# Kernel optimization log

Hardware: AMD Instinct MI355X
Metric: run time of the kernel (lower is better)

The kernel has to match this reference:

```python
import jax, jax.numpy as jnp
import numpy as np

B, N, C_IN = 4, 2048, 64
HID, HEADS, NQ = 128, 4, 16
D = HID // HEADS  # per-head dim = 32
NEG_SLOPE = 0.2
MASK_VAL = -1e9


def setup_inputs() -> dict:
    key = jax.random.key(0)
    ks = jax.random.split(key, 8)
    x = jax.random.normal(ks[0], (B, N, C_IN), dtype=jnp.float32)
    adj = jax.random.randint(ks[1], (N, N), 0, 2, dtype=jnp.int32)
    # lin_in: Linear(in_channels, hidden_dim)
    W_in = jax.random.normal(ks[2], (C_IN, HID), dtype=jnp.float32) / np.sqrt(C_IN)
    b_in = jnp.zeros((HID,), dtype=jnp.float32)
    # attention vectors [1, heads, d]
    att_src = jax.random.normal(ks[3], (1, HEADS, D), dtype=jnp.float32) * 0.1
    att_dst = jax.random.normal(ks[4], (1, HEADS, D), dtype=jnp.float32) * 0.1
    # output_head: Linear(num_nodes*hidden_dim, num_qubits)
    W_out = jax.random.normal(ks[5], (N * HID, NQ), dtype=jnp.float32) / np.sqrt(N * HID)
    b_out = jnp.zeros((NQ,), dtype=jnp.float32)
    return {"x": x, "adj": adj, "W_in": W_in, "b_in": b_in,
            "att_src": att_src, "att_dst": att_dst,
            "W_out": W_out, "b_out": b_out}


def reference(x, adj, W_in, b_in, att_src, att_dst, W_out, b_out):
    b, n, _ = x.shape
    h = (x @ W_in + b_in).reshape(b, n, HEADS, D)          # [B,N,H,D]
    alpha_src = jnp.sum(h * att_src, axis=-1)               # [B,N,H]
    alpha_dst = jnp.sum(h * att_dst, axis=-1)               # [B,N,H]
    # additive scores: score[b,i,j,h] = src[b,i,h] + dst[b,j,h]
    scores = alpha_src[:, :, None, :] + alpha_dst[:, None, :, :]  # [B,N,N,H]
    scores = jnp.where(scores >= 0, scores, NEG_SLOPE * scores)   # leaky relu
    mask = (adj == 0)[None, :, :, None]                     # [1,N,N,1]
    scores = jnp.where(mask, MASK_VAL, scores)
    alpha = jax.nn.softmax(scores, axis=2)                  # softmax over neighbors j
    # dropout p=0.0 (eval) -> identity
    out = jnp.einsum('bijh,bjhd->bihd', alpha, h)           # [B,N,H,D]
    out = out.reshape(b, n * HEADS * D)                     # [B, N*HID]
    return out @ W_out + b_out                              # [B, NQ]
```

## Files before the change

kernel.cpp:

```cpp
#include <hip/hip_runtime.h>
#include <math.h>

#define BB 4
#define NN 2048
#define CIN 64
#define HID 128
#define HEADS 4
#define NQ 16
#define KTOT (NN*HID)
#define LOG2E 1.44269504088896340736f
#define NEGBIG_BITS 0xC2C80000u
#define NSL 2

typedef __attribute__((ext_vector_type(8))) _Float16 half8;
typedef __attribute__((ext_vector_type(2))) _Float16 half2;
typedef __attribute__((ext_vector_type(4))) float f32x4;
typedef __attribute__((ext_vector_type(4))) unsigned uint4v;

#define GLDS16(g, l) __builtin_amdgcn_global_load_lds((const __attribute__((address_space(1))) unsigned int*)(g), (__attribute__((address_space(3))) unsigned int*)(l), 16, 0, 0)

__global__ __launch_bounds__(256) void k_hidden(
    const float* __restrict__ x, const float* __restrict__ W_in,
    const float* __restrict__ b_in, const float* __restrict__ att_src,
    const float* __restrict__ att_dst, _Float16* __restrict__ hH,
    float* __restrict__ srcA, float* __restrict__ dstA)
{
    __shared__ float Wl[CIN * HID];
    __shared__ float xl[16][CIN];
    const int t = threadIdx.x;
    const int jj0 = blockIdx.x * 16;

    {
        const float4* Ws = (const float4*)W_in;
        float4* Wd = (float4*)Wl;
#pragma unroll
        for (int u = 0; u < 8; ++u) Wd[t + 256 * u] = Ws[t + 256 * u];
        ((float4*)&xl[0][0])[t] = ((const float4*)(x + (size_t)jj0 * CIN))[t];
    }
    __syncthreads();

    const int c = t & 127, rg = t >> 7;
    const int b = jj0 >> 11, j0 = (jj0 & (NN - 1)) + rg * 8;
    const int h = c >> 5;

    float acc[8];
    const float bc = b_in[c];
#pragma unroll
    for (int rr = 0; rr < 8; ++rr) acc[rr] = bc;

#pragma unroll
    for (int k4 = 0; k4 < CIN; k4 += 4) {
        const float w0 = Wl[(k4 + 0) * HID + c];
        const float w1 = Wl[(k4 + 1) * HID + c];
        const float w2 = Wl[(k4 + 2) * HID + c];
        const float w3 = Wl[(k4 + 3) * HID + c];
#pragma unroll
        for (int rr = 0; rr < 8; ++rr) {
            const float4 xv = *(const float4*)&xl[rg * 8 + rr][k4];
            acc[rr] = fmaf(xv.w, w3, fmaf(xv.z, w2, fmaf(xv.y, w1, fmaf(xv.x, w0, acc[rr]))));
        }
    }

    half8 hv;
#pragma unroll
    for (int rr = 0; rr < 8; ++rr) hv[rr] = (_Float16)acc[rr];
    *(half8*)(hH + (size_t)(b * HID + c) * NN + j0) = hv;

    const float as = att_src[c], ad = att_dst[c];
#pragma unroll
    for (int rr = 0; rr < 8; ++rr) {
        float vs = acc[rr] * as, vd = acc[rr] * ad;
#pragma unroll
        for (int m = 16; m >= 1; m >>= 1) {
            vs += __shfl_xor(vs, m, 64);
            vd += __shfl_xor(vd, m, 64);
        }
        if ((t & 31) == 0) {
            srcA[(size_t)(b * HEADS + h) * NN + j0 + rr] = vs * LOG2E;
            dstA[(size_t)(b * HEADS + h) * NN + j0 + rr] = vd * LOG2E;
        }
    }
}

__global__ __launch_bounds__(256) void k_adjb(const int* __restrict__ adj,
                                              unsigned* __restrict__ adjb,
                                              const float* __restrict__ b_out,
                                              float* __restrict__ dout)
{
    const int t = threadIdx.x;
    if (blockIdx.x == 0 && t < 64) dout[t] = b_out[t & 15];
    const int gid = blockIdx.x * 256 + t;
    const int lane = t & 63;
    const int4* p = (const int4*)(adj + (size_t)gid * 8);
    const int4 a = p[0], b = p[1];
    unsigned byte =
        (a.x != 0 ? 1u : 0u)  | (a.y != 0 ? 2u : 0u)  | (a.z != 0 ? 4u : 0u)  | (a.w != 0 ? 8u : 0u) |
        (b.x != 0 ? 16u : 0u) | (b.y != 0 ? 32u : 0u) | (b.z != 0 ? 64u : 0u) | (b.w != 0 ? 128u : 0u);
    unsigned u = byte | (((unsigned)__shfl_xor((int)byte, 1, 64)) << 8);
    u = u | (((unsigned)__shfl_xor((int)u, 2, 64)) << 16);
    if ((lane & 3) == 0) adjb[gid >> 2] = u;
}

__global__ __launch_bounds__(256, 4) void k_attn(
    const unsigned* __restrict__ adjb, const _Float16* __restrict__ hH,
    const float* __restrict__ srcA, const float* __restrict__ dstA,
    float* __restrict__ P, float* __restrict__ S)
{
    __shared__ __align__(16) char sm[4 * 8192];

    const int t = threadIdx.x;
    const int lane = t & 63;
    const int w = t >> 6;
    const int h = w;
    const int bx = blockIdx.x;
    const int ih = bx & 1;
    const int it = (bx >> 1) & 63;
    const int b = (bx >> 7) & 3;
    const int jh = bx >> 9;
    const int i0 = it * 32;
    const int jbase = jh * 1024;

    const int r16 = lane & 15;
    const int g = lane >> 4;
    const int sw16 = (r16 & 7) << 4;

    char* mybuf = sm + w * 8192;
    const _Float16* hrow = hH + ((size_t)(b * HID) + h * 32) * NN;
    const float srci = srcA[(size_t)(b * HEADS + h) * NN + i0 + ih * 16 + r16];
    const uint2* adjr = (const uint2*)(adjb + (size_t)(i0 + ih * 16 + r16) * (NN / 32)) + (jbase >> 6);
    const float4* dstt = (const float4*)(dstA + (size_t)(b * HEADS + h) * NN + jbase);

    const int srow = lane >> 3;
    const int sj8 = (lane & 7) ^ srow;
    auto STAGE = [&](int buf, int n) {
        const int jt = jbase + n * 64;
        const _Float16* gsrc = hrow + (size_t)srow * NN + jt + sj8 * 8;
        char* ldst = mybuf + buf * 4096;
#pragma unroll
        for (int u = 0; u < 4; ++u)
            GLDS16(gsrc + (size_t)(u * 8) * NN, ldst + u * 1024);
    };

    f32x4 acc0 = {0.f, 0.f, 0.f, 0.f};
    f32x4 acc1 = {0.f, 0.f, 0.f, 0.f};
    f32x4 accS = {0.f, 0.f, 0.f, 0.f};
    const half8 ones = {(_Float16)1.f, (_Float16)1.f, (_Float16)1.f, (_Float16)1.f,
                        (_Float16)1.f, (_Float16)1.f, (_Float16)1.f, (_Float16)1.f};

    STAGE(0, 0);
    asm volatile("s_waitcnt vmcnt(0)" ::: "memory");

    int buf = 0;
#pragma unroll 1
    for (int n = 0; n < 16; ++n) {
        if (n + 1 < 16) STAGE(buf ^ 1, n + 1);

        const uint2 aw = adjr[n];
        const char* hb = mybuf + buf * 4096;

#pragma unroll
        for (int jg = 0; jg < 2; ++jg) {
            const int cb = jg * 64 + g * 16;
            const half8 bb0 = *(const half8*)(hb + r16 * 128 + (cb ^ sw16));
            const half8 bb1 = *(const half8*)(hb + (16 + r16) * 128 + (cb ^ sw16));
            const float4 dv0 = dstt[n * 16 + jg * 8 + g * 2];
            const float4 dv1 = dstt[n * 16 + jg * 8 + g * 2 + 1];
            const unsigned bits = (jg ? aw.y : aw.x) >> (8 * g);
            const float dvv[8] = {dv0.x, dv0.y, dv0.z, dv0.w, dv1.x, dv1.y, dv1.z, dv1.w};
            float wv[8];
#pragma unroll
            for (int e = 0; e < 8; ++e) {
                float s = srci + dvv[e];
                s = fmaxf(s, 0.2f * s);
                const unsigned m = (unsigned)(((int)(bits << (31 - e))) >> 31);
                const unsigned su = __builtin_bit_cast(unsigned, s);
                wv[e] = __builtin_amdgcn_exp2f(
                    __builtin_bit_cast(float, (su & m) | (NEGBIG_BITS & ~m)));
            }
            uint4v uu;
            uu[0] = __builtin_bit_cast(unsigned, __builtin_amdgcn_cvt_pkrtz(wv[0], wv[1]));
            uu[1] = __builtin_bit_cast(unsigned, __builtin_amdgcn_cvt_pkrtz(wv[2], wv[3]));
            uu[2] = __builtin_bit_cast(unsigned, __builtin_amdgcn_cvt_pkrtz(wv[4], wv[5]));
            uu[3] = __builtin_bit_cast(unsigned, __builtin_amdgcn_cvt_pkrtz(wv[6], wv[7]));
            const half8 af = __builtin_bit_cast(half8, uu);
            acc0 = __builtin_amdgcn_mfma_f32_16x16x32_f16(af, bb0, acc0, 0, 0, 0);
            acc1 = __builtin_amdgcn_mfma_f32_16x16x32_f16(af, bb1, acc1, 0, 0, 0);
            accS = __builtin_amdgcn_mfma_f32_16x16x32_f16(af, ones, accS, 0, 0, 0);
        }

        asm volatile("s_waitcnt vmcnt(0)" ::: "memory");
        buf ^= 1;
    }

    const size_t prow0 = (size_t)(jh * BB + b) * NN + i0 + ih * 16;
#pragma unroll
    for (int r = 0; r < 4; ++r) {
        const size_t row = prow0 + 4 * g + r;
        P[row * HID + h * 32 + r16]      = acc0[r];
        P[row * HID + h * 32 + 16 + r16] = acc1[r];
        if (r16 == 0) S[row * HEADS + h] = accS[r];
    }
}

__global__ __launch_bounds__(256) void k_proj(
    const float* __restrict__ P, const float* __restrict__ S,
    const float* __restrict__ W_out, float* __restrict__ dout)
{
    __shared__ float wlT[NQ][260];
    __shared__ float red[256];

    const int t = threadIdx.x;
    const int k0 = blockIdx.x * 256;

#pragma unroll
    for (int u = 0; u < 4; ++u) {
        const int flat = (u * 256 + t) * 4;
        const float4 wv = *(const float4*)(W_out + (size_t)k0 * NQ + flat);
        const int krel = flat >> 4;
        const int q0 = flat & 15;
        wlT[q0 + 0][krel] = wv.x;
        wlT[q0 + 1][krel] = wv.y;
        wlT[q0 + 2][krel] = wv.z;
        wlT[q0 + 3][krel] = wv.w;
    }
    __syncthreads();

    const int q = t & 15;
    const int b = (t >> 4) & 3;
    const int ks = (t >> 6) * 64;
    const int i = (k0 + ks) >> 7;

    const float* p0 = P + (size_t)b * KTOT + k0 + ks;
    const float* p1 = P + (size_t)(BB + b) * KTOT + k0 + ks;

    float acc = 0.f;
#pragma unroll
    for (int seg = 0; seg < 2; ++seg) {
        const int h = ((k0 + ks + seg * 32) >> 5) & 3;
        const float rs = S[((size_t)b * NN + i) * HEADS + h] +
                         S[((size_t)(BB + b) * NN + i) * HEADS + h];
        const float inv = __builtin_amdgcn_rcpf(rs);
#pragma unroll
        for (int k4 = 0; k4 < 8; ++k4) {
            const int kk = seg * 32 + k4 * 4;
            const float4 a0 = *(const float4*)(p0 + kk);
            const float4 a1 = *(const float4*)(p1 + kk);
            const float4 wq = *(const float4*)&wlT[q][ks + kk];
            acc = fmaf((a0.x + a1.x) * inv, wq.x, acc);
            acc = fmaf((a0.y + a1.y) * inv, wq.y, acc);
            acc = fmaf((a0.z + a1.z) * inv, wq.z, acc);
            acc = fmaf((a0.w + a1.w) * inv, wq.w, acc);
        }
    }

    red[t] = acc;
    __syncthreads();
    if (t < 64)
        atomicAdd(&dout[t], red[t] + red[t + 64] + red[t + 128] + red[t + 192]);
}

extern "C" void kernel_launch(void* const* d_in, const int* in_sizes, int n_in,
                              void* d_out, int out_size, void* d_ws, size_t ws_size,
                              hipStream_t stream)
{
    const float* x       = (const float*)d_in[0];
    const int*   adj     = (const int*)d_in[1];
    const float* W_in    = (const float*)d_in[2];
    const float* b_in    = (const float*)d_in[3];
    const float* att_src = (const float*)d_in[4];
    const float* att_dst = (const float*)d_in[5];
    const float* W_out   = (const float*)d_in[6];
    const float* b_out   = (const float*)d_in[7];
    float* out = (float*)d_out;

    float* P    = (float*)d_ws;
    float* S    = P + (size_t)NSL * BB * KTOT;
    float* srcA = S + (size_t)NSL * BB * NN * HEADS;
    float* dstA = srcA + (size_t)BB * HEADS * NN;
    _Float16* hH = (_Float16*)(dstA + (size_t)BB * HEADS * NN);
    unsigned* adjbw = (unsigned*)((char*)hH + sizeof(_Float16) * (size_t)BB * KTOT);

    k_hidden<<<BB * NN / 16, 256, 0, stream>>>(x, W_in, b_in, att_src, att_dst, hH, srcA, dstA);
    k_adjb<<<NN * NN / 8 / 256, 256, 0, stream>>>(adj, adjbw, b_out, out);
    k_attn<<<NSL * BB * (NN / 32) * 2, 256, 0, stream>>>(adjbw, hH, srcA, dstA, P, S);
    k_proj<<<KTOT / 256, 256, 0, stream>>>(P, S, W_out, out);
}
```

Before: 77.76 us.

## Drop LDS staging in attention kernel, load B directly, split neighbors into four slices

The attention kernel no longer double-buffers h tiles through LDS with global_load_lds. Each lane now reads its half8 operands straight from global memory, with one 32-column j step per iteration. The neighbor dimension is split into four slices of 512 instead of two of 1024, occupancy is raised to 8 blocks per SM, and the grid grows accordingly. The projection kernel sums four partial P and S slices. This removes LDS traffic and waitcnt stalls and gains parallelism, but it relies on the cache for reuse, adds uncoalesced-ish global loads, and doubles the P/S workspace traffic in k_proj.

```diff
diff --git a/kernel.cpp b/kernel.cpp
--- a/kernel.cpp
+++ b/kernel.cpp
@@ -10,14 +10,11 @@
 #define KTOT (NN*HID)
 #define LOG2E 1.44269504088896340736f
 #define NEGBIG_BITS 0xC2C80000u
-#define NSL 2
+#define NSL 4
 
 typedef __attribute__((ext_vector_type(8))) _Float16 half8;
-typedef __attribute__((ext_vector_type(2))) _Float16 half2;
 typedef __attribute__((ext_vector_type(4))) float f32x4;
 typedef __attribute__((ext_vector_type(4))) unsigned uint4v;
-
-#define GLDS16(g, l) __builtin_amdgcn_global_load_lds((const __attribute__((address_space(1))) unsigned int*)(g), (__attribute__((address_space(3))) unsigned int*)(l), 16, 0, 0)
 
 __global__ __launch_bounds__(256) void k_hidden(
     const float* __restrict__ x, const float* __restrict__ W_in,
@@ -101,45 +98,29 @@
     if ((lane & 3) == 0) adjb[gid >> 2] = u;
 }
 
-__global__ __launch_bounds__(256, 4) void k_attn(
+__global__ __launch_bounds__(256, 8) void k_attn(
     const unsigned* __restrict__ adjb, const _Float16* __restrict__ hH,
     const float* __restrict__ srcA, const float* __restrict__ dstA,
     float* __restrict__ P, float* __restrict__ S)
 {
-    __shared__ __align__(16) char sm[4 * 8192];
-
     const int t = threadIdx.x;
     const int lane = t & 63;
-    const int w = t >> 6;
-    const int h = w;
+    const int h = t >> 6;
     const int bx = blockIdx.x;
-    const int ih = bx & 1;
-    const int it = (bx >> 1) & 63;
+    const int iq = bx & 127;
     const int b = (bx >> 7) & 3;
-    const int jh = bx >> 9;
-    const int i0 = it * 32;
-    const int jbase = jh * 1024;
+    const int jq = bx >> 9;
+    const int i0 = iq * 16;
+    const int jbase = jq * 512;
 
     const int r16 = lane & 15;
     const int g = lane >> 4;
-    const int sw16 = (r16 & 7) << 4;
-
-    char* mybuf = sm + w * 8192;
-    const _Float16* hrow = hH + ((size_t)(b * HID) + h * 32) * NN;
-    const float srci = srcA[(size_t)(b * HEADS + h) * NN + i0 + ih * 16 + r16];
-    const uint2* adjr = (const uint2*)(adjb + (size_t)(i0 + ih * 16 + r16) * (NN / 32)) + (jbase >> 6);
-    const float4* dstt = (const float4*)(dstA + (size_t)(b * HEADS + h) * NN + jbase);
-
-    const int srow = lane >> 3;
-    const int sj8 = (lane & 7) ^ srow;
-    auto STAGE = [&](int buf, int n) {
-        const int jt = jbase + n * 64;
-        const _Float16* gsrc = hrow + (size_t)srow * NN + jt + sj8 * 8;
-        char* ldst = mybuf + buf * 4096;
-#pragma unroll
-        for (int u = 0; u < 4; ++u)
-            GLDS16(gsrc + (size_t)(u * 8) * NN, ldst + u * 1024);
-    };
+
+    const float srci = srcA[(size_t)(b * HEADS + h) * NN + i0 + r16];
+    const unsigned* adjr = adjb + (size_t)(i0 + r16) * (NN / 32) + (jbase >> 5);
+    const _Float16* bbase0 = hH + ((size_t)(b * HID) + h * 32 + r16) * NN + jbase + 8 * g;
+    const _Float16* bbase1 = bbase0 + (size_t)16 * NN;
+    const float4* dst4 = (const float4*)(dstA + (size_t)(b * HEADS + h) * NN + jbase) + 2 * g;
 
     f32x4 acc0 = {0.f, 0.f, 0.f, 0.f};
     f32x4 acc1 = {0.f, 0.f, 0.f, 0.f};
@@ -147,52 +128,38 @@
     const half8 ones = {(_Float16)1.f, (_Float16)1.f, (_Float16)1.f, (_Float16)1.f,
                         (_Float16)1.f, (_Float16)1.f, (_Float16)1.f, (_Float16)1.f};
 
-    STAGE(0, 0);
-    asm volatile("s_waitcnt vmcnt(0)" ::: "memory");
-
-    int buf = 0;
 #pragma unroll 1
     for (int n = 0; n < 16; ++n) {
-        if (n + 1 < 16) STAGE(buf ^ 1, n + 1);
-
-        const uint2 aw = adjr[n];
-        const char* hb = mybuf + buf * 4096;
-
-#pragma unroll
-        for (int jg = 0; jg < 2; ++jg) {
-            const int cb = jg * 64 + g * 16;
-            const half8 bb0 = *(const half8*)(hb + r16 * 128 + (cb ^ sw16));
-            const half8 bb1 = *(const half8*)(hb + (16 + r16) * 128 + (cb ^ sw16));
-            const float4 dv0 = dstt[n * 16 + jg * 8 + g * 2];
-            const float4 dv1 = dstt[n * 16 + jg * 8 + g * 2 + 1];
-            const unsigned bits = (jg ? aw.y : aw.x) >> (8 * g);
-            const float dvv[8] = {dv0.x, dv0.y, dv0.z, dv0.w, dv1.x, dv1.y, dv1.z, dv1.w};
-            float wv[8];
-#pragma unroll
-            for (int e = 0; e < 8; ++e) {
-                float s = srci + dvv[e];
-                s = fmaxf(s, 0.2f * s);
-                const unsigned m = (unsigned)(((int)(bits << (31 - e))) >> 31);
-                const unsigned su = __builtin_bit_cast(unsigned, s);
-                wv[e] = __builtin_amdgcn_exp2f(
-                    __builtin_bit_cast(float, (su & m) | (NEGBIG_BITS & ~m)));
-            }
-            uint4v uu;
-            uu[0] = __builtin_bit_cast(unsigned, __builtin_amdgcn_cvt_pkrtz(wv[0], wv[1]));
-            uu[1] = __builtin_bit_cast(unsigned, __builtin_amdgcn_cvt_pkrtz(wv[2], wv[3]));
-            uu[2] = __builtin_bit_cast(unsigned, __builtin_amdgcn_cvt_pkrtz(wv[4], wv[5]));
-            uu[3] = __builtin_bit_cast(unsigned, __builtin_amdgcn_cvt_pkrtz(wv[6], wv[7]));
-            const half8 af = __builtin_bit_cast(half8, uu);
-            acc0 = __builtin_amdgcn_mfma_f32_16x16x32_f16(af, bb0, acc0, 0, 0, 0);
-            acc1 = __builtin_amdgcn_mfma_f32_16x16x32_f16(af, bb1, acc1, 0, 0, 0);
-            accS = __builtin_amdgcn_mfma_f32_16x16x32_f16(af, ones, accS, 0, 0, 0);
-        }
-
-        asm volatile("s_waitcnt vmcnt(0)" ::: "memory");
-        buf ^= 1;
-    }
-
-    const size_t prow0 = (size_t)(jh * BB + b) * NN + i0 + ih * 16;
+        const unsigned word = adjr[n];
+        const half8 bb0 = *(const half8*)(bbase0 + n * 32);
+        const half8 bb1 = *(const half8*)(bbase1 + n * 32);
+        const float4 dv0 = dst4[n * 8];
+        const float4 dv1 = dst4[n * 8 + 1];
+
+        const unsigned bits = word >> (8 * g);
+        const float dvv[8] = {dv0.x, dv0.y, dv0.z, dv0.w, dv1.x, dv1.y, dv1.z, dv1.w};
+        float wv[8];
+#pragma unroll
+        for (int e = 0; e < 8; ++e) {
+            float s = srci + dvv[e];
+            s = fmaxf(s, 0.2f * s);
+            const unsigned m = (unsigned)(((int)(bits << (31 - e))) >> 31);
+            const unsigned su = __builtin_bit_cast(unsigned, s);
+            wv[e] = __builtin_amdgcn_exp2f(
+                __builtin_bit_cast(float, (su & m) | (NEGBIG_BITS & ~m)));
+        }
+        uint4v uu;
+        uu[0] = __builtin_bit_cast(unsigned, __builtin_amdgcn_cvt_pkrtz(wv[0], wv[1]));
+        uu[1] = __builtin_bit_cast(unsigned, __builtin_amdgcn_cvt_pkrtz(wv[2], wv[3]));
+        uu[2] = __builtin_bit_cast(unsigned, __builtin_amdgcn_cvt_pkrtz(wv[4], wv[5]));
+        uu[3] = __builtin_bit_cast(unsigned, __builtin_amdgcn_cvt_pkrtz(wv[6], wv[7]));
+        const half8 af = __builtin_bit_cast(half8, uu);
+        acc0 = __builtin_amdgcn_mfma_f32_16x16x32_f16(af, bb0, acc0, 0, 0, 0);
+        acc1 = __builtin_amdgcn_mfma_f32_16x16x32_f16(af, bb1, acc1, 0, 0, 0);
+        accS = __builtin_amdgcn_mfma_f32_16x16x32_f16(af, ones, accS, 0, 0, 0);
+    }
+
+    const size_t prow0 = (size_t)(jq * BB + b) * NN + i0;
 #pragma unroll
     for (int r = 0; r < 4; ++r) {
         const size_t row = prow0 + 4 * g + r;
@@ -230,26 +197,32 @@
     const int ks = (t >> 6) * 64;
     const int i = (k0 + ks) >> 7;
 
-    const float* p0 = P + (size_t)b * KTOT + k0 + ks;
-    const float* p1 = P + (size_t)(BB + b) * KTOT + k0 + ks;
+    const float* p0 = P + (size_t)(0 * BB + b) * KTOT + k0 + ks;
+    const float* p1 = P + (size_t)(1 * BB + b) * KTOT + k0 + ks;
+    const float* p2 = P + (size_t)(2 * BB + b) * KTOT + k0 + ks;
+    const float* p3 = P + (size_t)(3 * BB + b) * KTOT + k0 + ks;
 
     float acc = 0.f;
 #pragma unroll
     for (int seg = 0; seg < 2; ++seg) {
         const int h = ((k0 + ks + seg * 32) >> 5) & 3;
-        const float rs = S[((size_t)b * NN + i) * HEADS + h] +
-                         S[((size_t)(BB + b) * NN + i) * HEADS + h];
+        float rs = 0.f;
+#pragma unroll
+        for (int s = 0; s < NSL; ++s)
+            rs += S[((size_t)(s * BB + b) * NN + i) * HEADS + h];
         const float inv = __builtin_amdgcn_rcpf(rs);
 #pragma unroll
         for (int k4 = 0; k4 < 8; ++k4) {
             const int kk = seg * 32 + k4 * 4;
             const float4 a0 = *(const float4*)(p0 + kk);
             const float4 a1 = *(const float4*)(p1 + kk);
+            const float4 a2 = *(const float4*)(p2 + kk);
+            const float4 a3 = *(const float4*)(p3 + kk);
             const float4 wq = *(const float4*)&wlT[q][ks + kk];
-            acc = fmaf((a0.x + a1.x) * inv, wq.x, acc);
-            acc = fmaf((a0.y + a1.y) * inv, wq.y, acc);
-            acc = fmaf((a0.z + a1.z) * inv, wq.z, acc);
-            acc = fmaf((a0.w + a1.w) * inv, wq.w, acc);
+            acc = fmaf(((a0.x + a1.x) + (a2.x + a3.x)) * inv, wq.x, acc);
+            acc = fmaf(((a0.y + a1.y) + (a2.y + a3.y)) * inv, wq.y, acc);
+            acc = fmaf(((a0.z + a1.z) + (a2.z + a3.z)) * inv, wq.z, acc);
+            acc = fmaf(((a0.w + a1.w) + (a2.w + a3.w)) * inv, wq.w, acc);
         }
     }
 
@@ -282,6 +255,6 @@
 
     k_hidden<<<BB * NN / 16, 256, 0, stream>>>(x, W_in, b_in, att_src, att_dst, hH, srcA, dstA);
     k_adjb<<<NN * NN / 8 / 256, 256, 0, stream>>>(adj, adjbw, b_out, out);
-    k_attn<<<NSL * BB * (NN / 32) * 2, 256, 0, stream>>>(adjbw, hH, srcA, dstA, P, S);
+    k_attn<<<NSL * BB * (NN / 16), 256, 0, stream>>>(adjbw, hH, srcA, dstA, P, S);
     k_proj<<<KTOT / 256, 256, 0, stream>>>(P, S, W_out, out);
 }
```

Result: slower. 105.8 us (+36.0%).
